# Performance work log

Measured on AMD Instinct MI355X. Metric: run time of the kernel, lower is better.

The kernel has to match this reference:

```python
import jax, jax.numpy as jnp
import numpy as np

B, T, NIN, N, NOUT = 64, 512, 64, 1024, 32
DT, TAU = 1.0, 10.0
STATE_STD, RATE_STD, OUT_STD = 0.05, 0.05, 0.05
HIDDEN_G = 1.0


def retanh(x):
    return jnp.maximum(jnp.tanh(x), 0.0)


def setup_inputs() -> dict:
    key = jax.random.key(0)
    ks = jax.random.split(key, 10)
    u = jax.random.normal(ks[0], (B, T, NIN), jnp.float32)
    x_0 = jnp.zeros((N,), jnp.float32)
    state_noise = STATE_STD * jax.random.normal(ks[1], (B, T, N), jnp.float32)
    rate_noise = RATE_STD * jax.random.normal(ks[2], (B, T, N), jnp.float32)
    output_noise = OUT_STD * jax.random.normal(ks[3], (B, T, NOUT), jnp.float32)
    W_in = jax.random.normal(ks[4], (N, NIN), jnp.float32) / np.sqrt(NIN).astype(np.float32)
    b_in = 0.1 + 0.01 * jax.random.normal(ks[5], (N,), jnp.float32)
    W_rec = jax.random.normal(ks[6], (N, N), jnp.float32) * (HIDDEN_G / np.sqrt(N).astype(np.float32))
    W_rec = W_rec * (1.0 - jnp.eye(N, dtype=jnp.float32))  # zero self-connections
    lim = 1.0 / np.sqrt(N).astype(np.float32)
    W_out = jax.random.uniform(ks[7], (NOUT, N), jnp.float32, -lim, lim)
    b_out = jax.random.uniform(ks[8], (NOUT,), jnp.float32, -lim, lim)
    return {"u": u, "x_0": x_0, "state_noise": state_noise, "rate_noise": rate_noise,
            "output_noise": output_noise, "W_in": W_in, "b_in": b_in, "W_rec": W_rec,
            "W_out": W_out, "b_out": b_out}


def reference(u, x_0, state_noise, rate_noise, output_noise, W_in, b_in, W_rec, W_out, b_out):
    alpha = DT / TAU
    # time-major for scan: [T, B, ...]
    u_t = jnp.swapaxes(u, 0, 1)
    sn = jnp.swapaxes(state_noise, 0, 1)
    rn = jnp.swapaxes(rate_noise, 0, 1)
    on = jnp.swapaxes(output_noise, 0, 1)
    x0 = jnp.broadcast_to(x_0, (B, N))
    r0 = retanh(x0)

    def step(carry, inp):
        x, r = carry
        ut, snt, rnt, ont = inp
        x_next = x + alpha * (-x + r @ W_rec.T + ut @ W_in.T + b_in + snt)
        r_next = retanh(x_next) + rnt
        z_next = r_next @ W_out.T + b_out + ont
        return (x_next, r_next), (x_next, r_next, z_next)

    _, (X, R, Z) = jax.lax.scan(step, (x0, r0), (u_t, sn, rn, on))
    # back to batch-major [B, T, ...]
    return (jnp.swapaxes(X, 0, 1), jnp.swapaxes(R, 0, 1), jnp.swapaxes(Z, 0, 1))
```

## Files before the change

### kernel.cpp

```cpp
#include <hip/hip_runtime.h>
#include <hip/hip_bf16.h>
#include <stdint.h>

#define B_    64
#define T_    512
#define NIN_  64
#define N_    1024
#define NOUT_ 32

#define NISL  16
#define BPI   16
#define MB    4
#define COLS  64
#define NT    4
#define KW    256
#define KT    8

#define MAIL_WORDS (NISL * BPI * BPI)

typedef float f32x4 __attribute__((ext_vector_type(4)));
typedef short s16x8 __attribute__((ext_vector_type(8)));

__device__ __forceinline__ unsigned short f2bf(float f) {
  union { float f; unsigned u; } v; v.f = f;
  unsigned r = v.u + 0x7FFFu + ((v.u >> 16) & 1u);
  return (unsigned short)(r >> 16);
}

__device__ __forceinline__ s16x8 cvt8(float4 a, float4 b) {
  s16x8 f;
  f[0] = (short)f2bf(a.x); f[1] = (short)f2bf(a.y);
  f[2] = (short)f2bf(a.z); f[3] = (short)f2bf(a.w);
  f[4] = (short)f2bf(b.x); f[5] = (short)f2bf(b.y);
  f[6] = (short)f2bf(b.z); f[7] = (short)f2bf(b.w);
  return f;
}

#define LD16S(dst, base, OFF) \
  asm volatile("global_load_dwordx4 %0, %1, off offset:" #OFF " sc0 sc1" \
               : "=v"(dst) : "v"(base) : "memory")
#define LDALLS() do { \
  LD16S(afr[0], bp, 0);   LD16S(afr[1], bp, 64);  \
  LD16S(afr[2], bp, 128); LD16S(afr[3], bp, 192); \
  LD16S(afr[4], bp, 256); LD16S(afr[5], bp, 320); \
  LD16S(afr[6], bp, 384); LD16S(afr[7], bp, 448); } while (0)

__global__ __launch_bounds__(256, 1) void rnn_scan(
    const float* __restrict__ U, const float* __restrict__ X0,
    const float* __restrict__ SN, const float* __restrict__ RN,
    const float* __restrict__ Wi, const float* __restrict__ Bi,
    const float* __restrict__ Wr,
    float* __restrict__ X, float* __restrict__ R,
    unsigned* __restrict__ mail, unsigned* __restrict__ ex)
{
  const int bid   = blockIdx.x;
  const int isl   = bid / BPI, slice = bid % BPI;
  const int tid   = threadIdx.x;
  const int wave  = tid >> 6, lane = tid & 63;
  const int l15   = lane & 15, koct = lane >> 4;
  const int colbase = slice * COLS;

  s16x8 bfrag[KT][NT];
#pragma unroll
  for (int kt = 0; kt < KT; ++kt) {
    const int k0 = wave * KW + kt * 32 + koct * 8;
#pragma unroll
    for (int nt = 0; nt < NT; ++nt) {
      const float4* q = (const float4*)(Wr + (size_t)(colbase + nt * 16 + l15) * N_ + k0);
      bfrag[kt][nt] = cvt8(q[0], q[1]);
    }
  }
  s16x8 wifrag[NT];
  if (wave < 2) {
#pragma unroll
    for (int nt = 0; nt < NT; ++nt) {
      const float4* q = (const float4*)(Wi + (size_t)(colbase + nt * 16 + l15) * NIN_ + wave * 32 + koct * 8);
      wifrag[nt] = cvt8(q[0], q[1]);
    }
  }

  const int cc   = lane;
  const int bloc = wave;
  const int bg   = isl * MB + bloc;
  const int nn   = colbase + cc;
  const int abatch = isl * MB + (l15 & 3);

  float x = X0[nn];
  const float bin = Bi[nn];
  const float r0 = fmaxf(tanhf(x), 0.f);

  const float* SNp = SN + (size_t)bg * T_ * N_ + nn;
  const float* RNp = RN + (size_t)bg * T_ * N_ + nn;
  float*       Xp  = X  + (size_t)bg * T_ * N_ + nn;
  float*       Rp  = R  + (size_t)bg * T_ * N_ + nn;
  const float* Up  = U  + (size_t)(isl * MB + (l15 & 3)) * T_ * NIN_ + wave * 32 + koct * 8;

  __shared__ float part[4][COLS][MB];

  const unsigned* const myline = mail + (isl * BPI + slice) * BPI;
  unsigned* const postcol      = mail + isl * BPI * BPI + slice;

  {
    unsigned short h = f2bf(r0);
    unsigned other = __shfl_xor((unsigned)h, 1);
    unsigned vv  = (unsigned)h | (other << 16);
    unsigned vv2 = __shfl_xor(vv, 2);
    if ((lane & 3) == 0) {
      uint64_t q8 = (uint64_t)vv | ((uint64_t)vv2 << 32);
      __hip_atomic_store((uint64_t*)(ex + (size_t)bg * (N_ / 2) + (nn >> 1)), q8,
                         __ATOMIC_RELAXED, __HIP_MEMORY_SCOPE_AGENT);
    }
  }
  __syncthreads();
  if (tid < BPI)
    __hip_atomic_store(postcol + tid * BPI, 1u,
                       __ATOMIC_RELAXED, __HIP_MEMORY_SCOPE_AGENT);

  float sn_c = SNp[0], rn_c = RNp[0];
  float4 uc0{}, uc1{};
  if (wave < 2) { const float4* q = (const float4*)Up; uc0 = q[0]; uc1 = q[1]; }

  for (int t = 0; t < T_; ++t) {
    const int par = t & 1;

    {
      const unsigned need = (unsigned)(t + 1);
      for (;;) {
        unsigned fv = __hip_atomic_load(myline + l15, __ATOMIC_RELAXED,
                                        __HIP_MEMORY_SCOPE_AGENT);
        if (__all((int)(fv >= need))) break;
        __builtin_amdgcn_s_sleep(1);
      }
    }

    const unsigned* bp = ex + (size_t)par * (B_ * (N_ / 2))
                            + (size_t)abatch * (N_ / 2)
                            + ((wave * KW + koct * 8) >> 1);
    s16x8 afr[KT];
    LDALLS();
    asm volatile("s_waitcnt vmcnt(0)" ::: "memory");
    __builtin_amdgcn_sched_barrier(0);

    f32x4 acc[NT];
#pragma unroll
    for (int nt = 0; nt < NT; ++nt) acc[nt] = f32x4{0.f, 0.f, 0.f, 0.f};
#pragma unroll
    for (int kt = 0; kt < KT; ++kt)
#pragma unroll
      for (int nt = 0; nt < NT; ++nt)
        acc[nt] = __builtin_amdgcn_mfma_f32_16x16x32_bf16(afr[kt], bfrag[kt][nt], acc[nt], 0, 0, 0);
    if (wave < 2) {
      s16x8 ua = cvt8(uc0, uc1);
#pragma unroll
      for (int nt = 0; nt < NT; ++nt)
        acc[nt] = __builtin_amdgcn_mfma_f32_16x16x32_bf16(ua, wifrag[nt], acc[nt], 0, 0, 0);
    }

    if (lane < 16) {
#pragma unroll
      for (int nt = 0; nt < NT; ++nt) {
        const int s = (nt * 2 + (lane >> 3)) & 3;
        f32x4 a = acc[nt];
        if (s & 1) a = f32x4{a[1], a[0], a[3], a[2]};
        if (s & 2) a = f32x4{a[2], a[3], a[0], a[1]};
        *(f32x4*)&part[wave][nt * 16 + lane][0] = a;
      }
    }
    __syncthreads();
    const int sr = (cc >> 3) & 3;
    const float mat = part[0][cc][bloc ^ sr] + part[1][cc][bloc ^ sr] +
                      part[2][cc][bloc ^ sr] + part[3][cc][bloc ^ sr];
    const float xn = x + 0.1f * (-x + mat + bin + sn_c);
    const float rv = fmaxf(tanhf(xn), 0.f) + rn_c;
    x = xn;

    {
      unsigned short h = f2bf(rv);
      unsigned other = __shfl_xor((unsigned)h, 1);
      unsigned vv  = (unsigned)h | (other << 16);
      unsigned vv2 = __shfl_xor(vv, 2);
      if ((lane & 3) == 0) {
        uint64_t q8 = (uint64_t)vv | ((uint64_t)vv2 << 32);
        __hip_atomic_store((uint64_t*)(ex + (size_t)(par ^ 1) * (B_ * (N_ / 2)) +
                                       (size_t)bg * (N_ / 2) + (nn >> 1)), q8,
                           __ATOMIC_RELAXED, __HIP_MEMORY_SCOPE_AGENT);
      }
    }
    __syncthreads();
    if (tid < BPI)
      __hip_atomic_store(postcol + tid * BPI, (unsigned)(t + 2),
                         __ATOMIC_RELAXED, __HIP_MEMORY_SCOPE_AGENT);

    Xp[(size_t)t * N_] = xn;
    Rp[(size_t)t * N_] = rv;
    if (t + 1 < T_) {
      sn_c = SNp[(size_t)(t + 1) * N_];
      rn_c = RNp[(size_t)(t + 1) * N_];
      if (wave < 2) {
        const float4* q = (const float4*)(Up + (size_t)(t + 1) * NIN_);
        uc0 = q[0]; uc1 = q[1];
      }
    }
  }
}

#define TCH 64
__global__ __launch_bounds__(256, 2) void rnn_zout(
    const float* __restrict__ Rm, const float* __restrict__ ON,
    const float* __restrict__ Wo, const float* __restrict__ Bo,
    float* __restrict__ Z)
{
  const int bid = blockIdx.x;
  const int b = bid >> 3, tq = bid & 7;
  const int tid = threadIdx.x;
  const int o = tid & 31, kc = tid >> 5;

  float4 wv[32];
  const float4* wp = (const float4*)(Wo + (size_t)o * N_ + kc * 128);
#pragma unroll
  for (int i = 0; i < 32; ++i) wv[i] = wp[i];
  const float bo = Bo[o];

  __shared__ float Rl[2][N_];
  __shared__ float zred[2][8][32];

  const int t0 = tq * TCH;
  ((float4*)Rl[0])[tid] = ((const float4*)(Rm + ((size_t)b * T_ + t0) * N_))[tid];
  __syncthreads();

  for (int i = 0; i < TCH; ++i) {
    const int cur = i & 1;
    const size_t row = (size_t)b * T_ + t0 + i;
    float4 nx;
    if (i + 1 < TCH)
      nx = ((const float4*)(Rm + (row + 1) * N_))[tid];
    float a0 = 0.f;
#pragma unroll
    for (int j = 0; j < 32; ++j) {
      const float* rp = &Rl[cur][kc * 128 + j * 4];
      a0 += wv[j].x * rp[0] + wv[j].y * rp[1] + wv[j].z * rp[2] + wv[j].w * rp[3];
    }
    if (i + 1 < TCH)
      ((float4*)Rl[cur ^ 1])[tid] = nx;
    zred[cur][kc][o] = a0;
    __syncthreads();
    if (tid < 32) {
      float z = bo;
#pragma unroll
      for (int k = 0; k < 8; ++k) z += zred[cur][k][tid];
      Z[row * NOUT_ + tid] = z + ON[row * NOUT_ + tid];
    }
  }
}

extern "C" void kernel_launch(void* const* d_in, const int* in_sizes, int n_in,
                              void* d_out, int out_size, void* d_ws, size_t ws_size,
                              hipStream_t stream) {
  const float* U  = (const float*)d_in[0];
  const float* X0 = (const float*)d_in[1];
  const float* SN = (const float*)d_in[2];
  const float* RN = (const float*)d_in[3];
  const float* ON = (const float*)d_in[4];
  const float* Wi = (const float*)d_in[5];
  const float* Bi = (const float*)d_in[6];
  const float* Wr = (const float*)d_in[7];
  const float* Wo = (const float*)d_in[8];
  const float* Bo = (const float*)d_in[9];

  float* X = (float*)d_out;
  float* R = X + (size_t)B_ * T_ * N_;
  float* Z = R + (size_t)B_ * T_ * N_;

  unsigned* mail = (unsigned*)d_ws;
  unsigned* ex   = (unsigned*)((char*)d_ws + 65536);

  hipMemsetAsync(mail, 0, MAIL_WORDS * sizeof(unsigned), stream);

  hipLaunchKernelGGL(rnn_scan, dim3(NISL * BPI), dim3(256), 0, stream,
                     U, X0, SN, RN, Wi, Bi, Wr, X, R, mail, ex);
  hipLaunchKernelGGL(rnn_zout, dim3(B_ * (T_ / TCH)), dim3(256), 0, stream,
                     R, ON, Wo, Bo, Z);
}
```

Measured before the change: 1.490 ms.

## Speculatively prefetch exchange buffer with parity tags embedded in bf16 LSBs

Each step's activation exchange loads are now issued right after the previous step's publish, so they overlap with output stores and the flag-polling wait. A parity tag is stored in the low mantissa bit of every bf16 value, and the buffer is pre-filled with 0xFF. When every loaded word carries the expected tag, the data is used without waiting first, and the flag wait is deferred until before the next publish. Otherwise the code falls back to polling and reloading. This trades one mantissa bit of precision and extra tag-check ALU work for lower latency on the inter-block synchronisation critical path.

```diff
diff --git a/kernel.cpp b/kernel.cpp
--- a/kernel.cpp
+++ b/kernel.cpp
@@ -17,6 +17,7 @@
 #define KT    8
 
 #define MAIL_WORDS (NISL * BPI * BPI)
+#define EX_WORDS   (2 * B_ * (N_ / 2))
 
 typedef float f32x4 __attribute__((ext_vector_type(4)));
 typedef short s16x8 __attribute__((ext_vector_type(8)));
@@ -39,11 +40,20 @@
 #define LD16S(dst, base, OFF) \
   asm volatile("global_load_dwordx4 %0, %1, off offset:" #OFF " sc0 sc1" \
                : "=v"(dst) : "v"(base) : "memory")
-#define LDALLS() do { \
-  LD16S(afr[0], bp, 0);   LD16S(afr[1], bp, 64);  \
-  LD16S(afr[2], bp, 128); LD16S(afr[3], bp, 192); \
-  LD16S(afr[4], bp, 256); LD16S(afr[5], bp, 320); \
-  LD16S(afr[6], bp, 384); LD16S(afr[7], bp, 448); } while (0)
+#define LDALLS(bpv) do { \
+  LD16S(afr[0], bpv, 0);   LD16S(afr[1], bpv, 64);  \
+  LD16S(afr[2], bpv, 128); LD16S(afr[3], bpv, 192); \
+  LD16S(afr[4], bpv, 256); LD16S(afr[5], bpv, 320); \
+  LD16S(afr[6], bpv, 384); LD16S(afr[7], bpv, 448); } while (0)
+#define TAGCHECK(okvar) do { \
+  unsigned bad_ = 0; \
+  _Pragma("unroll") \
+  for (int kt_ = 0; kt_ < KT; ++kt_) { \
+    union { s16x8 v; unsigned u[4]; } w_; w_.v = afr[kt_]; \
+    bad_ |= (w_.u[0] ^ tgm) | (w_.u[1] ^ tgm) | (w_.u[2] ^ tgm) | (w_.u[3] ^ tgm); \
+  } \
+  okvar = __all((int)((bad_ & 1u) == 0u)); \
+} while (0)
 
 __global__ __launch_bounds__(256, 1) void rnn_scan(
     const float* __restrict__ U, const float* __restrict__ X0,
@@ -100,46 +110,60 @@
   const unsigned* const myline = mail + (isl * BPI + slice) * BPI;
   unsigned* const postcol      = mail + isl * BPI * BPI + slice;
 
+  const int kofs = (wave * KW + koct * 8) >> 1;
+  const unsigned* const exb0 = ex + (size_t)abatch * (N_ / 2) + kofs;
+  const unsigned* const exb1 = exb0 + (size_t)B_ * (N_ / 2);
+  unsigned* const exw0 = ex + (size_t)bg * (N_ / 2) + (nn >> 1);
+  unsigned* const exw1 = exw0 + (size_t)B_ * (N_ / 2);
+
+  float sn_c = SNp[0], rn_c = RNp[0];
+  float4 uc0{}, uc1{};
+  if (wave < 2) { const float4* q = (const float4*)Up; uc0 = q[0]; uc1 = q[1]; }
+
   {
     unsigned short h = f2bf(r0);
     unsigned other = __shfl_xor((unsigned)h, 1);
-    unsigned vv  = (unsigned)h | (other << 16);
+    unsigned vv  = ((unsigned)h & ~1u) | (other << 16);
     unsigned vv2 = __shfl_xor(vv, 2);
     if ((lane & 3) == 0) {
       uint64_t q8 = (uint64_t)vv | ((uint64_t)vv2 << 32);
-      __hip_atomic_store((uint64_t*)(ex + (size_t)bg * (N_ / 2) + (nn >> 1)), q8,
-                         __ATOMIC_RELAXED, __HIP_MEMORY_SCOPE_AGENT);
+      __hip_atomic_store((uint64_t*)exw0, q8, __ATOMIC_RELAXED, __HIP_MEMORY_SCOPE_AGENT);
     }
   }
   __syncthreads();
   if (tid < BPI)
-    __hip_atomic_store(postcol + tid * BPI, 1u,
-                       __ATOMIC_RELAXED, __HIP_MEMORY_SCOPE_AGENT);
-
-  float sn_c = SNp[0], rn_c = RNp[0];
-  float4 uc0{}, uc1{};
-  if (wave < 2) { const float4* q = (const float4*)Up; uc0 = q[0]; uc1 = q[1]; }
+    __hip_atomic_store(postcol + tid * BPI, 1u, __ATOMIC_RELAXED, __HIP_MEMORY_SCOPE_AGENT);
+
+  s16x8 afr[KT];
+  LDALLS(exb0);
+  asm volatile("s_waitcnt vmcnt(0)" ::: "memory");
+  __builtin_amdgcn_sched_barrier(0);
 
   for (int t = 0; t < T_; ++t) {
-    const int par = t & 1;
-
-    {
-      const unsigned need = (unsigned)(t + 1);
-      for (;;) {
-        unsigned fv = __hip_atomic_load(myline + l15, __ATOMIC_RELAXED,
-                                        __HIP_MEMORY_SCOPE_AGENT);
-        if (__all((int)(fv >= need))) break;
-        __builtin_amdgcn_s_sleep(1);
-      }
-    }
-
-    const unsigned* bp = ex + (size_t)par * (B_ * (N_ / 2))
-                            + (size_t)abatch * (N_ / 2)
-                            + ((wave * KW + koct * 8) >> 1);
-    s16x8 afr[KT];
-    LDALLS();
-    asm volatile("s_waitcnt vmcnt(0)" ::: "memory");
+    const unsigned tgm = ((t >> 1) & 1) ? 0xFFFFFFFFu : 0u;
+    const unsigned need = (unsigned)(t + 1);
+
+    if (wave < 2) asm volatile("s_waitcnt vmcnt(5)" ::: "memory");
+    else          asm volatile("s_waitcnt vmcnt(4)" ::: "memory");
     __builtin_amdgcn_sched_barrier(0);
+    int ok; TAGCHECK(ok);
+
+    unsigned fv0 = __hip_atomic_load(myline + l15, __ATOMIC_RELAXED,
+                                     __HIP_MEMORY_SCOPE_AGENT);
+    if (!ok) {
+      if (!__all((int)(fv0 >= need))) {
+        for (;;) {
+          unsigned fv = __hip_atomic_load(myline + l15, __ATOMIC_RELAXED,
+                                          __HIP_MEMORY_SCOPE_AGENT);
+          if (__all((int)(fv >= need))) break;
+          __builtin_amdgcn_s_sleep(1);
+        }
+      }
+      const unsigned* bp = (t & 1) ? exb1 : exb0;
+      LDALLS(bp);
+      asm volatile("s_waitcnt vmcnt(0)" ::: "memory");
+      __builtin_amdgcn_sched_barrier(0);
+    }
 
     f32x4 acc[NT];
 #pragma unroll
@@ -174,15 +198,26 @@
     const float rv = fmaxf(tanhf(xn), 0.f) + rn_c;
     x = xn;
 
+    if (ok) {
+      if (!__all((int)(fv0 >= need))) {
+        for (;;) {
+          unsigned fv = __hip_atomic_load(myline + l15, __ATOMIC_RELAXED,
+                                          __HIP_MEMORY_SCOPE_AGENT);
+          if (__all((int)(fv >= need))) break;
+          __builtin_amdgcn_s_sleep(1);
+        }
+      }
+    }
+
     {
+      const unsigned tgn = ((t + 1) >> 1) & 1;
       unsigned short h = f2bf(rv);
       unsigned other = __shfl_xor((unsigned)h, 1);
-      unsigned vv  = (unsigned)h | (other << 16);
+      unsigned vv  = (((unsigned)h & ~1u) | tgn) | (other << 16);
       unsigned vv2 = __shfl_xor(vv, 2);
       if ((lane & 3) == 0) {
         uint64_t q8 = (uint64_t)vv | ((uint64_t)vv2 << 32);
-        __hip_atomic_store((uint64_t*)(ex + (size_t)(par ^ 1) * (B_ * (N_ / 2)) +
-                                       (size_t)bg * (N_ / 2) + (nn >> 1)), q8,
+        __hip_atomic_store((uint64_t*)((t & 1) ? exw0 : exw1), q8,
                            __ATOMIC_RELAXED, __HIP_MEMORY_SCOPE_AGENT);
       }
     }
@@ -191,6 +226,10 @@
       __hip_atomic_store(postcol + tid * BPI, (unsigned)(t + 2),
                          __ATOMIC_RELAXED, __HIP_MEMORY_SCOPE_AGENT);
 
+    if (t + 1 < T_) {
+      const unsigned* bpn = ((t + 1) & 1) ? exb1 : exb0;
+      LDALLS(bpn);
+    }
     Xp[(size_t)t * N_] = xn;
     Rp[(size_t)t * N_] = rv;
     if (t + 1 < T_) {
@@ -275,6 +314,7 @@
   unsigned* ex   = (unsigned*)((char*)d_ws + 65536);
 
   hipMemsetAsync(mail, 0, MAIL_WORDS * sizeof(unsigned), stream);
+  hipMemsetAsync(ex, 0xFF, EX_WORDS * sizeof(unsigned), stream);
 
   hipLaunchKernelGGL(rnn_scan, dim3(NISL * BPI), dim3(256), 0, stream,
                      U, X0, SN, RN, Wi, Bi, Wr, X, R, mail, ex);
```

Measured after the change: 1.742 ms. 1.17x slower.
